# Optimization experiments

Measured on AMD Instinct MI355X. Metric: run time of the kernel, lower is better.

The kernel has to match this reference:

```python
import jax, jax.numpy as jnp
import numpy as np

D_MODEL = 1024
N_HEADS = 16
HEAD_DIM = D_MODEL // N_HEADS
B, LQ, LK = 4, 2048, 2048


def _rope(x, cos, sin):
    # x: (B, H, L, d); cos/sin: (B, 1, L, d)
    d = x.shape[-1]
    x1, x2 = x[..., : d // 2], x[..., d // 2 :]
    rotated = jnp.concatenate([-x2, x1], axis=-1)
    return x * cos + rotated * sin


def setup_inputs() -> dict:
    key = jax.random.key(0)
    ks = jax.random.split(key, 16)
    s = 1.0 / np.sqrt(D_MODEL)
    inp = {
        "query": jax.random.normal(ks[0], (B, LQ, D_MODEL), jnp.float32),
        "key": jax.random.normal(ks[1], (B, LK, D_MODEL), jnp.float32),
        "value": jax.random.normal(ks[2], (B, LK, D_MODEL), jnp.float32),
        "cos_q": jax.random.normal(ks[3], (B, LQ, HEAD_DIM), jnp.float32),
        "sin_q": jax.random.normal(ks[4], (B, LQ, HEAD_DIM), jnp.float32),
        "cos_k": jax.random.normal(ks[5], (B, LK, HEAD_DIM), jnp.float32),
        "sin_k": jax.random.normal(ks[6], (B, LK, HEAD_DIM), jnp.float32),
        "key_padding_mask": jnp.zeros((B, LK), dtype=bool),
        "Wq": jax.random.normal(ks[7], (D_MODEL, D_MODEL), jnp.float32) * s,
        "bq": jnp.zeros((D_MODEL,), jnp.float32),
        "Wk": jax.random.normal(ks[8], (D_MODEL, D_MODEL), jnp.float32) * s,
        "bk": jnp.zeros((D_MODEL,), jnp.float32),
        "Wv": jax.random.normal(ks[9], (D_MODEL, D_MODEL), jnp.float32) * s,
        "bv": jnp.zeros((D_MODEL,), jnp.float32),
        "Wo": jax.random.normal(ks[10], (D_MODEL, D_MODEL), jnp.float32) * s,
        "bo": jnp.zeros((D_MODEL,), jnp.float32),
    }
    return inp


def reference(query, key, value, cos_q, sin_q, cos_k, sin_k, key_padding_mask,
              Wq, bq, Wk, bk, Wv, bv, Wo, bo):
    Bq, Lq, _ = query.shape
    Lk = key.shape[1]
    scale = HEAD_DIM ** -0.5

    def proj(x, W, b, L):
        # torch Linear: x @ W.T + b, then (B, L, H, d) -> (B, H, L, d)
        y = jnp.einsum('ble,de->bld', x, W) + b
        return y.reshape(Bq, L, N_HEADS, HEAD_DIM).transpose(0, 2, 1, 3)

    q = proj(query, Wq, bq, Lq)
    k = proj(key, Wk, bk, Lk)
    v = proj(value, Wv, bv, Lk)

    q = _rope(q, cos_q[:, None, :Lq, :HEAD_DIM], sin_q[:, None, :Lq, :HEAD_DIM])
    k = _rope(k, cos_k[:, None, :Lk, :HEAD_DIM], sin_k[:, None, :Lk, :HEAD_DIM])

    attn = jnp.einsum('bhqd,bhkd->bhqk', q, k) * scale
    attn = jnp.where(key_padding_mask[:, None, None, :], -jnp.inf, attn)
    attn = jax.nn.softmax(attn, axis=-1)

    out = jnp.einsum('bhqk,bhkd->bhqd', attn, v)
    out = out.transpose(0, 2, 1, 3).reshape(Bq, Lq, D_MODEL)
    return jnp.einsum('ble,de->bld', out, Wo) + bo
```

## Files before the change

### kernel.cpp

```cpp
#include <hip/hip_runtime.h>
#include <hip/hip_bf16.h>
#include <stdint.h>
#include <stddef.h>

#define B_DIM 4
#define NH    16
#define LSEQ  2048
#define HD    64
#define DM    1024
#define TOKENS (B_DIM * LSEQ)

typedef __bf16 bf16_t;
typedef __attribute__((ext_vector_type(8))) __bf16 bf16x8;
typedef __attribute__((ext_vector_type(4))) __bf16 bf16x4;
typedef __attribute__((ext_vector_type(4))) float  f32x4;

#define GLD16(gp, lp) \
  __builtin_amdgcn_global_load_lds((__attribute__((address_space(1))) void*)(gp), \
                                   (__attribute__((address_space(3))) void*)(lp), 16, 0, 0)

__device__ __forceinline__ f32x4 mfma_16x16x32(bf16x8 a, bf16x8 b, f32x4 c) {
  return __builtin_amdgcn_mfma_f32_16x16x32_bf16(a, b, c, 0, 0, 0);
}

__global__ __launch_bounds__(256) void cast3_kernel(const float* __restrict__ a,
                                                    const float* __restrict__ b,
                                                    const float* __restrict__ c,
                                                    bf16_t* __restrict__ dst, int n) {
  const float* src = (blockIdx.y == 0) ? a : (blockIdx.y == 1) ? b : c;
  const int i = (blockIdx.x * 256 + threadIdx.x) * 4;
  if (i < n) {
    const float4 v = *(const float4*)(src + i);
    bf16x4 o;
    o[0] = (bf16_t)v.x; o[1] = (bf16_t)v.y; o[2] = (bf16_t)v.z; o[3] = (bf16_t)v.w;
    *(bf16x4*)(dst + (size_t)blockIdx.y * n + i) = o;
  }
}

__global__ __launch_bounds__(256) void cast4_kernel(const float* __restrict__ a,
                                                    const float* __restrict__ b,
                                                    const float* __restrict__ c,
                                                    const float* __restrict__ d,
                                                    bf16_t* __restrict__ dst, int n) {
  const float* src = (blockIdx.y == 0) ? a : (blockIdx.y == 1) ? b
                   : (blockIdx.y == 2) ? c : d;
  const int i = (blockIdx.x * 256 + threadIdx.x) * 4;
  if (i < n) {
    const float4 v = *(const float4*)(src + i);
    bf16x4 o;
    o[0] = (bf16_t)v.x; o[1] = (bf16_t)v.y; o[2] = (bf16_t)v.z; o[3] = (bf16_t)v.w;
    *(bf16x4*)(dst + (size_t)blockIdx.y * n + i) = o;
  }
}

__global__ __launch_bounds__(256) void qkv_proj_kernel(const bf16_t* __restrict__ X,
                                                       const bf16_t* __restrict__ Wb,
                                                       const float* __restrict__ bq,
                                                       const float* __restrict__ bk,
                                                       const float* __restrict__ bv,
                                                       const float* __restrict__ cos_q,
                                                       const float* __restrict__ sin_q,
                                                       const float* __restrict__ cos_k,
                                                       const float* __restrict__ sin_k,
                                                       bf16_t* __restrict__ qtb,
                                                       bf16_t* __restrict__ ktb,
                                                       bf16_t* __restrict__ vtb) {
  __shared__ bf16_t As[128 * 32];
  __shared__ bf16_t Bs[128 * 32];
  const int z = blockIdx.z;
  const bf16_t* A  = X  + (size_t)z * TOKENS * DM;
  const bf16_t* Bw = Wb + (size_t)z * DM * DM;
  const float* bias = (z == 0) ? bq : (z == 1) ? bk : bv;

  const int tid  = threadIdx.x;
  const int wave = tid >> 6, lane = tid & 63;
  const int quad = lane >> 4, l16 = lane & 15;
  const int m0 = blockIdx.x * 128, n0 = blockIdx.y * 128;
  const int wm = (wave >> 1) * 64, wn = (wave & 1) * 64;

  f32x4 acc[4][4];
#pragma unroll
  for (int i = 0; i < 4; ++i)
#pragma unroll
    for (int j = 0; j < 4; ++j) acc[i][j] = (f32x4){0.f, 0.f, 0.f, 0.f};

  const int srow = lane >> 2;
  const int scol = (lane & 3) * 8;

  for (int kk = 0; kk < DM; kk += 32) {
    __syncthreads();
#pragma unroll
    for (int t = 0; t < 2; ++t) {
      const int c   = wave * 2 + t;
      const int row = c * 16 + srow;
      GLD16(A  + (size_t)(m0 + row) * DM + kk + scol, As + c * 512);
      GLD16(Bw + (size_t)(n0 + row) * DM + kk + scol, Bs + c * 512);
    }
    __syncthreads();
    bf16x8 af[4], bfr[4];
#pragma unroll
    for (int i = 0; i < 4; ++i)
      af[i] = *(const bf16x8*)(As + (wm + i * 16 + l16) * 32 + quad * 8);
#pragma unroll
    for (int j = 0; j < 4; ++j)
      bfr[j] = *(const bf16x8*)(Bs + (wn + j * 16 + l16) * 32 + quad * 8);
#pragma unroll
    for (int i = 0; i < 4; ++i)
#pragma unroll
      for (int j = 0; j < 4; ++j)
        acc[i][j] = mfma_16x16x32(af[i], bfr[j], acc[i][j]);
  }

  if (z < 2) {
    const float* cosb = (z == 0) ? cos_q : cos_k;
    const float* sinb = (z == 0) ? sin_q : sin_k;
    bf16_t* out = (z == 0) ? qtb : ktb;
    const int h = (n0 + wn) >> 6;
#pragma unroll
    for (int i = 0; i < 4; ++i) {
#pragma unroll
      for (int j = 0; j < 2; ++j) {
        const int hd1 = j * 16 + l16;
        const int hd2 = hd1 + 32;
        const float bn1 = bias[n0 + wn + hd1];
        const float bn2 = bias[n0 + wn + hd2];
#pragma unroll
        for (int r = 0; r < 4; ++r) {
          const int m = m0 + wm + i * 16 + quad * 4 + r;
          const int b = m >> 11, l = m & (LSEQ - 1);
          const size_t cb = ((size_t)b * LSEQ + l) * HD;
          const float x1 = (float)(bf16_t)(acc[i][j][r] + bn1);
          const float x2 = (float)(bf16_t)(acc[i][j + 2][r] + bn2);
          const float c1 = cosb[cb + hd1], s1 = sinb[cb + hd1];
          const float c2 = cosb[cb + hd2], s2 = sinb[cb + hd2];
          bf16_t* dst = out + (((size_t)(b * NH + h)) * LSEQ + l) * HD;
          dst[hd1] = (bf16_t)(x1 * c1 - x2 * s1);
          dst[hd2] = (bf16_t)(x2 * c2 + x1 * s2);
        }
      }
    }
  } else {
#pragma unroll
    for (int i = 0; i < 4; ++i) {
      const int mb = m0 + wm + i * 16 + quad * 4;
      const int b = mb >> 11, l = mb & (LSEQ - 1);
#pragma unroll
      for (int j = 0; j < 4; ++j) {
        const int n = n0 + wn + j * 16 + l16;
        const int h = n >> 6, hd = n & (HD - 1);
        const float bn = bias[n];
        bf16x4 pk;
#pragma unroll
        for (int r = 0; r < 4; ++r) pk[r] = (bf16_t)(acc[i][j][r] + bn);
        *(bf16x4*)(vtb + (((size_t)(b * NH + h)) * HD + hd) * LSEQ + l) = pk;
      }
    }
  }
}

__global__ __launch_bounds__(256) void out_gemm_kernel(const bf16_t* __restrict__ A,
                                                       const bf16_t* __restrict__ Bw,
                                                       const float* __restrict__ bias,
                                                       float* __restrict__ out) {
  __shared__ bf16_t As[128 * 32];
  __shared__ bf16_t Bs[128 * 32];
  const int tid  = threadIdx.x;
  const int wave = tid >> 6, lane = tid & 63;
  const int quad = lane >> 4, l16 = lane & 15;
  const int m0 = blockIdx.x * 128, n0 = blockIdx.y * 128;
  const int wm = (wave >> 1) * 64, wn = (wave & 1) * 64;

  f32x4 acc[4][4];
#pragma unroll
  for (int i = 0; i < 4; ++i)
#pragma unroll
    for (int j = 0; j < 4; ++j) acc[i][j] = (f32x4){0.f, 0.f, 0.f, 0.f};

  const int srow = lane >> 2;
  const int scol = (lane & 3) * 8;

  for (int kk = 0; kk < DM; kk += 32) {
    __syncthreads();
#pragma unroll
    for (int t = 0; t < 2; ++t) {
      const int c   = wave * 2 + t;
      const int row = c * 16 + srow;
      GLD16(A  + (size_t)(m0 + row) * DM + kk + scol, As + c * 512);
      GLD16(Bw + (size_t)(n0 + row) * DM + kk + scol, Bs + c * 512);
    }
    __syncthreads();
    bf16x8 af[4], bfr[4];
#pragma unroll
    for (int i = 0; i < 4; ++i)
      af[i] = *(const bf16x8*)(As + (wm + i * 16 + l16) * 32 + quad * 8);
#pragma unroll
    for (int j = 0; j < 4; ++j)
      bfr[j] = *(const bf16x8*)(Bs + (wn + j * 16 + l16) * 32 + quad * 8);
#pragma unroll
    for (int i = 0; i < 4; ++i)
#pragma unroll
      for (int j = 0; j < 4; ++j)
        acc[i][j] = mfma_16x16x32(af[i], bfr[j], acc[i][j]);
  }

#pragma unroll
  for (int i = 0; i < 4; ++i)
#pragma unroll
    for (int j = 0; j < 4; ++j) {
      const int n  = n0 + wn + j * 16 + l16;
      const float bn = bias[n];
#pragma unroll
      for (int r = 0; r < 4; ++r) {
        const int m = m0 + wm + i * 16 + quad * 4 + r;
        out[(size_t)m * DM + n] = acc[i][j][r] + bn;
      }
    }
}

__global__ __launch_bounds__(256, 4) void attn_kernel(const bf16_t* __restrict__ qt,
                                                      const bf16_t* __restrict__ kt,
                                                      const bf16_t* __restrict__ vt,
                                                      const unsigned char* __restrict__ mask,
                                                      bf16_t* __restrict__ ctx) {
  __shared__ bf16_t Kl[2][64 * 64];
  __shared__ bf16_t Vl[2][64 * 64];
  __shared__ int mflag;
  const int bh = blockIdx.y;
  const int b = bh >> 4, h = bh & (NH - 1);
  const int q0 = blockIdx.x * 128;
  const int tid = threadIdx.x;
  const int wave = tid >> 6, lane = tid & 63;
  const int quad = lane >> 4, l16 = lane & 15;
  const float scale_l2e = 0.125f * 1.44269504f;

  const bf16_t* kbase = kt + (size_t)bh * LSEQ * HD;
  const bf16_t* vbase = vt + (size_t)bh * HD * LSEQ;
  const unsigned char* mrow = mask + (size_t)b * LSEQ;

  if (tid == 0) mflag = 0;
  __syncthreads();
  {
    const uint64_t mw = ((const uint64_t*)mrow)[tid];
    if (mw != 0) atomicOr(&mflag, 1);
  }

  bf16x8 qa[2][2];
#pragma unroll
  for (int u = 0; u < 2; ++u) {
    const bf16_t* qrow = qt + (((size_t)bh * LSEQ) + q0 + wave * 32 + u * 16 + l16) * HD;
    qa[u][0] = *(const bf16x8*)(qrow + quad * 8);
    qa[u][1] = *(const bf16x8*)(qrow + 32 + quad * 8);
  }

  f32x4 O[2][4];
  f32x4 Ol[2];
#pragma unroll
  for (int u = 0; u < 2; ++u) {
    Ol[u] = (f32x4){0.f, 0.f, 0.f, 0.f};
#pragma unroll
    for (int j = 0; j < 4; ++j) O[u][j] = (f32x4){0.f, 0.f, 0.f, 0.f};
  }
  bf16x8 ones;
#pragma unroll
  for (int e = 0; e < 8; ++e) ones[e] = (bf16_t)1.0f;

  const int srow8 = lane >> 3;
  const int scb   = lane & 7;
  const int c0 = wave * 2, c1 = c0 + 1;
  const int p0 = c0 * 8 + srow8, p1 = p0 + 8;
  const int g0 = (scb ^ srow8) * 8;
  const int sig0 = ((p0 >> 5) << 5) | (((p0 >> 2) & 3) << 3) | (((p0 >> 4) & 1) << 2) | (p0 & 3);
  const int sig1 = ((p1 >> 5) << 5) | (((p1 >> 2) & 3) << 3) | (((p1 >> 4) & 1) << 2) | (p1 & 3);
  const int kgo0 = sig0 * HD + g0, kgo1 = sig1 * HD + g0;
  const int vgo0 = p0 * LSEQ + g0, vgo1 = p1 * LSEQ + g0;
  const int ld0 = c0 * 512, ld1 = c1 * 512;

  const int sw  = l16 & 7;
  const int oA  = l16 * 64 + ((quad ^ sw) << 3);
  const int oB  = l16 * 64 + (((quad + 4) ^ sw) << 3);

  GLD16(kbase + kgo0, &Kl[0][0] + ld0);
  GLD16(kbase + kgo1, &Kl[0][0] + ld1);
  GLD16(vbase + vgo0, &Vl[0][0] + ld0);
  GLD16(vbase + vgo1, &Vl[0][0] + ld1);
  __syncthreads();
  const bool has_mask = (mflag != 0);

  int cur = 0;
  for (int t = 0; t < 32; ++t) {
    const int k0 = t * 64;

    if (t < 31) {
      const int k0n = k0 + 64;
      bf16_t* Kd = &Kl[cur ^ 1][0];
      bf16_t* Vd = &Vl[cur ^ 1][0];
      GLD16(kbase + (size_t)k0n * HD + kgo0, Kd + ld0);
      GLD16(kbase + (size_t)k0n * HD + kgo1, Kd + ld1);
      GLD16(vbase + (size_t)(vgo0 + k0n), Vd + ld0);
      GLD16(vbase + (size_t)(vgo1 + k0n), Vd + ld1);
    }

    const bf16_t* Kc = &Kl[cur][0];
    const bf16_t* Vc = &Vl[cur][0];

    f32x4 S[2][4];
#pragma unroll
    for (int j = 0; j < 4; ++j) {
      const bf16x8 kb0 = *(const bf16x8*)(Kc + oA + j * 1024);
      const bf16x8 kb1 = *(const bf16x8*)(Kc + oB + j * 1024);
#pragma unroll
      for (int u = 0; u < 2; ++u) {
        f32x4 a = (f32x4){0.f, 0.f, 0.f, 0.f};
        a = mfma_16x16x32(kb0, qa[u][0], a);
        a = mfma_16x16x32(kb1, qa[u][1], a);
#pragma unroll
        for (int r = 0; r < 4; ++r)
          S[u][j][r] = __builtin_amdgcn_exp2f(a[r] * scale_l2e);
      }
    }

    if (has_mask) {
      const uint64_t mlo = *(const uint64_t*)(mrow + k0 + quad * 8);
      const uint64_t mhi = *(const uint64_t*)(mrow + k0 + 32 + quad * 8);
      if (!__all((mlo | mhi) == 0)) {
#pragma unroll
        for (int j = 0; j < 4; ++j) {
          const uint64_t mm = (j & 2) ? mhi : mlo;
#pragma unroll
          for (int r = 0; r < 4; ++r)
            if ((mm >> (((j & 1) * 4 + r) * 8)) & 0xff) {
              S[0][j][r] = 0.f;
              S[1][j][r] = 0.f;
            }
        }
      }
    }

    bf16x8 pa[2][2];
#pragma unroll
    for (int u = 0; u < 2; ++u)
#pragma unroll
      for (int f = 0; f < 2; ++f)
#pragma unroll
        for (int e = 0; e < 8; ++e)
          pa[u][f][e] = (bf16_t)S[u][2 * f + (e >> 2)][e & 3];

#pragma unroll
    for (int u = 0; u < 2; ++u) {
      Ol[u] = mfma_16x16x32(pa[u][0], ones, Ol[u]);
      Ol[u] = mfma_16x16x32(pa[u][1], ones, Ol[u]);
    }

#pragma unroll
    for (int jd = 0; jd < 4; ++jd) {
      const bf16x8 vb0 = *(const bf16x8*)(Vc + oA + jd * 1024);
      const bf16x8 vb1 = *(const bf16x8*)(Vc + oB + jd * 1024);
#pragma unroll
      for (int u = 0; u < 2; ++u) {
        O[u][jd] = mfma_16x16x32(pa[u][0], vb0, O[u][jd]);
        O[u][jd] = mfma_16x16x32(pa[u][1], vb1, O[u][jd]);
      }
    }

    if (t < 31) __syncthreads();
    cur ^= 1;
  }

#pragma unroll
  for (int u = 0; u < 2; ++u) {
    f32x4 linv;
#pragma unroll
    for (int r = 0; r < 4; ++r) linv[r] = 1.0f / Ol[u][r];
#pragma unroll
    for (int jd = 0; jd < 4; ++jd)
#pragma unroll
      for (int r = 0; r < 4; ++r) {
        const int l = q0 + wave * 32 + u * 16 + quad * 4 + r;
        const int d = h * HD + jd * 16 + l16;
        const float o = O[u][jd][r] * linv[r];
        ctx[((size_t)b * LSEQ + l) * DM + d] = (bf16_t)o;
      }
  }
}

extern "C" void kernel_launch(void* const* d_in, const int* in_sizes, int n_in,
                              void* d_out, int out_size, void* d_ws, size_t ws_size,
                              hipStream_t stream) {
  (void)in_sizes; (void)n_in; (void)out_size; (void)ws_size;
  const float* query = (const float*)d_in[0];
  const float* key   = (const float*)d_in[1];
  const float* value = (const float*)d_in[2];
  const float* cos_q = (const float*)d_in[3];
  const float* sin_q = (const float*)d_in[4];
  const float* cos_k = (const float*)d_in[5];
  const float* sin_k = (const float*)d_in[6];
  const unsigned char* mask = (const unsigned char*)d_in[7];
  const float* Wq = (const float*)d_in[8];
  const float* bq = (const float*)d_in[9];
  const float* Wk = (const float*)d_in[10];
  const float* bk = (const float*)d_in[11];
  const float* Wv = (const float*)d_in[12];
  const float* bv = (const float*)d_in[13];
  const float* Wo = (const float*)d_in[14];
  const float* bo = (const float*)d_in[15];
  float* out = (float*)d_out;

  const size_t ACT = (size_t)TOKENS * DM;
  const size_t WEL = (size_t)DM * DM;

  bf16_t* p   = (bf16_t*)d_ws;
  bf16_t* xq  = p; p += ACT;
  bf16_t* xk  = p; p += ACT;
  bf16_t* xv  = p; p += ACT;
  bf16_t* wqb = p; p += WEL;
  bf16_t* wkb = p; p += WEL;
  bf16_t* wvb = p; p += WEL;
  bf16_t* wob = p; p += WEL;
  bf16_t* qtb = p; p += ACT;
  bf16_t* ktb = p; p += ACT;
  bf16_t* vtb = p; p += ACT;
  bf16_t* ctx = xk;
  (void)xv; (void)wkb; (void)wvb;

  cast3_kernel<<<dim3((int)(ACT / 1024), 3), 256, 0, stream>>>(query, key, value, xq, (int)ACT);
  cast4_kernel<<<dim3((int)(WEL / 1024), 4), 256, 0, stream>>>(Wq, Wk, Wv, Wo, wqb, (int)WEL);

  qkv_proj_kernel<<<dim3(TOKENS / 128, DM / 128, 3), 256, 0, stream>>>(
      xq, wqb, bq, bk, bv, cos_q, sin_q, cos_k, sin_k, qtb, ktb, vtb);

  attn_kernel<<<dim3(LSEQ / 128, B_DIM * NH), 256, 0, stream>>>(qtb, ktb, vtb, mask, ctx);

  out_gemm_kernel<<<dim3(TOKENS / 128, DM / 128), 256, 0, stream>>>(ctx, wob, bo, out);
}
```

Baseline: 365.7 us.

## Double-buffer LDS tiles and XOR-swizzle columns in projection GEMMs

Both the QKV projection and output projection GEMMs now keep two LDS buffers, so the global-to-LDS load for the next K slice is issued before the MFMAs on the current slice, and there is one barrier per iteration instead of two. LDS columns are also XOR-swizzled by row on both the store and fragment-read side to cut bank conflicts on the 16-byte fragment reads. This doubles LDS use per block, which may lower occupancy. Correctness depends on the global_load_lds completion being covered by the single syncthreads wait.

```diff
diff --git a/kernel.cpp b/kernel.cpp
--- a/kernel.cpp
+++ b/kernel.cpp
@@ -65,8 +65,8 @@
                                                        bf16_t* __restrict__ qtb,
                                                        bf16_t* __restrict__ ktb,
                                                        bf16_t* __restrict__ vtb) {
-  __shared__ bf16_t As[128 * 32];
-  __shared__ bf16_t Bs[128 * 32];
+  __shared__ bf16_t As[2][128 * 32];
+  __shared__ bf16_t Bs[2][128 * 32];
   const int z = blockIdx.z;
   const bf16_t* A  = X  + (size_t)z * TOKENS * DM;
   const bf16_t* Bw = Wb + (size_t)z * DM * DM;
@@ -85,30 +85,46 @@
     for (int j = 0; j < 4; ++j) acc[i][j] = (f32x4){0.f, 0.f, 0.f, 0.f};
 
   const int srow = lane >> 2;
-  const int scol = (lane & 3) * 8;
-
-  for (int kk = 0; kk < DM; kk += 32) {
-    __syncthreads();
-#pragma unroll
-    for (int t = 0; t < 2; ++t) {
-      const int c   = wave * 2 + t;
-      const int row = c * 16 + srow;
-      GLD16(A  + (size_t)(m0 + row) * DM + kk + scol, As + c * 512);
-      GLD16(Bw + (size_t)(n0 + row) * DM + kk + scol, Bs + c * 512);
-    }
-    __syncthreads();
+  const int scol = ((lane & 3) ^ ((lane >> 3) & 3)) * 8;
+  const int c0 = wave * 2, c1 = c0 + 1;
+  const int r0 = c0 * 16 + srow, r1 = c1 * 16 + srow;
+  const bf16_t* Ag0 = A  + (size_t)(m0 + r0) * DM + scol;
+  const bf16_t* Ag1 = A  + (size_t)(m0 + r1) * DM + scol;
+  const bf16_t* Bg0 = Bw + (size_t)(n0 + r0) * DM + scol;
+  const bf16_t* Bg1 = Bw + (size_t)(n0 + r1) * DM + scol;
+  const int ld0 = c0 * 512, ld1 = c1 * 512;
+
+  const int fcol = ((quad ^ ((l16 >> 1) & 3)) << 3);
+
+  GLD16(Ag0, &As[0][0] + ld0); GLD16(Ag1, &As[0][0] + ld1);
+  GLD16(Bg0, &Bs[0][0] + ld0); GLD16(Bg1, &Bs[0][0] + ld1);
+  __syncthreads();
+
+  int cur = 0;
+  for (int t = 0; t < 32; ++t) {
+    if (t < 31) {
+      const int kk = (t + 1) * 32;
+      bf16_t* Ad = &As[cur ^ 1][0];
+      bf16_t* Bd = &Bs[cur ^ 1][0];
+      GLD16(Ag0 + kk, Ad + ld0); GLD16(Ag1 + kk, Ad + ld1);
+      GLD16(Bg0 + kk, Bd + ld0); GLD16(Bg1 + kk, Bd + ld1);
+    }
+    const bf16_t* Ac = &As[cur][0];
+    const bf16_t* Bc = &Bs[cur][0];
     bf16x8 af[4], bfr[4];
 #pragma unroll
     for (int i = 0; i < 4; ++i)
-      af[i] = *(const bf16x8*)(As + (wm + i * 16 + l16) * 32 + quad * 8);
+      af[i] = *(const bf16x8*)(Ac + (wm + i * 16 + l16) * 32 + fcol);
 #pragma unroll
     for (int j = 0; j < 4; ++j)
-      bfr[j] = *(const bf16x8*)(Bs + (wn + j * 16 + l16) * 32 + quad * 8);
+      bfr[j] = *(const bf16x8*)(Bc + (wn + j * 16 + l16) * 32 + fcol);
 #pragma unroll
     for (int i = 0; i < 4; ++i)
 #pragma unroll
       for (int j = 0; j < 4; ++j)
         acc[i][j] = mfma_16x16x32(af[i], bfr[j], acc[i][j]);
+    if (t < 31) __syncthreads();
+    cur ^= 1;
   }
 
   if (z < 2) {
@@ -162,8 +178,8 @@
                                                        const bf16_t* __restrict__ Bw,
                                                        const float* __restrict__ bias,
                                                        float* __restrict__ out) {
-  __shared__ bf16_t As[128 * 32];
-  __shared__ bf16_t Bs[128 * 32];
+  __shared__ bf16_t As[2][128 * 32];
+  __shared__ bf16_t Bs[2][128 * 32];
   const int tid  = threadIdx.x;
   const int wave = tid >> 6, lane = tid & 63;
   const int quad = lane >> 4, l16 = lane & 15;
@@ -177,30 +193,45 @@
     for (int j = 0; j < 4; ++j) acc[i][j] = (f32x4){0.f, 0.f, 0.f, 0.f};
 
   const int srow = lane >> 2;
-  const int scol = (lane & 3) * 8;
-
-  for (int kk = 0; kk < DM; kk += 32) {
-    __syncthreads();
-#pragma unroll
-    for (int t = 0; t < 2; ++t) {
-      const int c   = wave * 2 + t;
-      const int row = c * 16 + srow;
-      GLD16(A  + (size_t)(m0 + row) * DM + kk + scol, As + c * 512);
-      GLD16(Bw + (size_t)(n0 + row) * DM + kk + scol, Bs + c * 512);
-    }
-    __syncthreads();
+  const int scol = ((lane & 3) ^ ((lane >> 3) & 3)) * 8;
+  const int c0 = wave * 2, c1 = c0 + 1;
+  const int r0 = c0 * 16 + srow, r1 = c1 * 16 + srow;
+  const bf16_t* Ag0 = A  + (size_t)(m0 + r0) * DM + scol;
+  const bf16_t* Ag1 = A  + (size_t)(m0 + r1) * DM + scol;
+  const bf16_t* Bg0 = Bw + (size_t)(n0 + r0) * DM + scol;
+  const bf16_t* Bg1 = Bw + (size_t)(n0 + r1) * DM + scol;
+  const int ld0 = c0 * 512, ld1 = c1 * 512;
+  const int fcol = ((quad ^ ((l16 >> 1) & 3)) << 3);
+
+  GLD16(Ag0, &As[0][0] + ld0); GLD16(Ag1, &As[0][0] + ld1);
+  GLD16(Bg0, &Bs[0][0] + ld0); GLD16(Bg1, &Bs[0][0] + ld1);
+  __syncthreads();
+
+  int cur = 0;
+  for (int t = 0; t < 32; ++t) {
+    if (t < 31) {
+      const int kk = (t + 1) * 32;
+      bf16_t* Ad = &As[cur ^ 1][0];
+      bf16_t* Bd = &Bs[cur ^ 1][0];
+      GLD16(Ag0 + kk, Ad + ld0); GLD16(Ag1 + kk, Ad + ld1);
+      GLD16(Bg0 + kk, Bd + ld0); GLD16(Bg1 + kk, Bd + ld1);
+    }
+    const bf16_t* Ac = &As[cur][0];
+    const bf16_t* Bc = &Bs[cur][0];
     bf16x8 af[4], bfr[4];
 #pragma unroll
     for (int i = 0; i < 4; ++i)
-      af[i] = *(const bf16x8*)(As + (wm + i * 16 + l16) * 32 + quad * 8);
+      af[i] = *(const bf16x8*)(Ac + (wm + i * 16 + l16) * 32 + fcol);
 #pragma unroll
     for (int j = 0; j < 4; ++j)
-      bfr[j] = *(const bf16x8*)(Bs + (wn + j * 16 + l16) * 32 + quad * 8);
+      bfr[j] = *(const bf16x8*)(Bc + (wn + j * 16 + l16) * 32 + fcol);
 #pragma unroll
     for (int i = 0; i < 4; ++i)
 #pragma unroll
       for (int j = 0; j < 4; ++j)
         acc[i][j] = mfma_16x16x32(af[i], bfr[j], acc[i][j]);
+    if (t < 31) __syncthreads();
+    cur ^= 1;
   }
 
 #pragma unroll
```

New measurement: 367.2 us. Within noise of the previous version (+0.4%).
